# Kernel tuning notes

Measured on AMD Instinct MI355X. Metric: run time of the kernel, lower is better.

Reference implementation:

```python
import math
import jax, jax.numpy as jnp
import numpy as np

EPS = 1e-6
MAX_SCALE_LOG = math.log(100.0)

def rms_norm(x, scale, eps=EPS):
    # x * scale / rms(x), reduction over last dim
    ms = jnp.mean(jnp.square(x), axis=-1, keepdims=True)
    return x * (scale * jax.lax.rsqrt(ms + eps))

def axial_rope_theta(pos, n_heads, d_head, dtype):
    # freqs: linspace in log-space from pi to 10*pi, reshaped to [n_heads, d_head//4]
    f = np.exp(np.linspace(math.log(math.pi), math.log(10.0 * math.pi),
                           n_heads * d_head // 4 + 1)[:-1])
    freqs = jnp.asarray(f.reshape(d_head // 4, n_heads).T, dtype)  # [h, e/4]
    theta_h = pos[:, :, None, 0:1] * freqs  # [n, l, h, e/4]
    theta_w = pos[:, :, None, 1:2] * freqs  # [n, l, h, e/4]
    theta = jnp.concatenate([theta_h, theta_w], axis=-1)  # [n, l, h, e/2]
    return theta.transpose(0, 2, 1, 3)  # [n, h, l, e/2]

def apply_rotary(x, theta):
    d = theta.shape[-1]
    x1, x2, x3 = x[..., :d], x[..., d:2 * d], x[..., 2 * d:]
    cos, sin = jnp.cos(theta), jnp.sin(theta)
    return jnp.concatenate([x1 * cos - x2 * sin, x2 * cos + x1 * sin, x3], axis=-1)

def setup_inputs() -> dict:
    key = jax.random.key(0)
    ks = jax.random.split(key, 8)
    n, l, d_model, d_head = 2, 2048, 1024, 64
    n_heads = d_model // d_head
    x = jax.random.normal(ks[0], (n, l, d_model), jnp.float32)
    pos = jax.random.uniform(ks[1], (n, l, 2), jnp.float32)
    cond = jax.random.normal(ks[2], (n, 1, d_model), jnp.float32)
    # params (torch uses zero-init for w_cond/w_out; small random for a non-degenerate baseline)
    w_cond = jax.random.normal(ks[3], (d_model, d_model), jnp.float32) * 0.02
    w_qkv = jax.random.normal(ks[4], (d_model, 3 * d_model), jnp.float32) * (d_model ** -0.5)
    qk_scale = jnp.full((n_heads,), math.log(10.0), jnp.float32)
    w_out = jax.random.normal(ks[5], (d_model, d_model), jnp.float32) * 0.02
    return {"x": x, "pos": pos, "cond": cond, "w_cond": w_cond,
            "w_qkv": w_qkv, "qk_scale": qk_scale, "w_out": w_out}

def reference(x, pos, cond, w_cond, w_qkv, qk_scale, w_out):
    n, l, d_model = x.shape
    h = qk_scale.shape[0]
    e = d_model // h
    # AdaRMSNorm: scale = linear(cond) + 1
    xn = rms_norm(x, cond @ w_cond + 1.0)
    # QKV projection
    q, k, v = jnp.split(xn @ w_qkv, 3, axis=-1)
    to_heads = lambda t: t.reshape(n, l, h, e).transpose(0, 2, 1, 3)  # [n,h,l,e]
    q, k, v = to_heads(q), to_heads(k), to_heads(v)
    # QKNorm: per-head learned scale, rms over head dim
    s = jnp.exp(0.5 * jnp.minimum(qk_scale, MAX_SCALE_LOG) - 0.25 * math.log(e))
    q = rms_norm(q, s[:, None, None])
    k = rms_norm(k, s[:, None, None])
    # Axial RoPE
    theta = axial_rope_theta(pos, h, e, x.dtype)
    q = apply_rotary(q, theta)
    k = apply_rotary(k, theta)
    # SDPA (no mask)
    attn = jax.nn.softmax(jnp.einsum('nhqe,nhke->nhqk', q, k) / math.sqrt(e), axis=-1)
    o = jnp.einsum('nhqk,nhke->nhqe', attn, v)
    o = o.transpose(0, 2, 1, 3).reshape(n, l, d_model)
    return o @ w_out
```

## Files before the change

### kernel.cpp

```cpp
#include <hip/hip_runtime.h>

typedef unsigned short u16;
typedef unsigned int u32;
typedef short s16x8 __attribute__((ext_vector_type(8)));
typedef short s16x4 __attribute__((ext_vector_type(4)));
typedef float f32x4 __attribute__((ext_vector_type(4)));
typedef float f32x16 __attribute__((ext_vector_type(16)));

#define AS1 __attribute__((address_space(1)))
#define AS3 __attribute__((address_space(3)))

__device__ __forceinline__ float bf2f(u16 u) {
    union { unsigned int i; float f; } x; x.i = ((unsigned int)u) << 16; return x.f;
}
__device__ __forceinline__ u16 f2bf(float f) {
    union { float f; unsigned int i; } x; x.f = f;
    unsigned int r = (x.i + 0x7FFFu + ((x.i >> 16) & 1u)) >> 16;
    return (u16)r;
}
__device__ __forceinline__ void storeOut(u16* p, float v) { *p = f2bf(v); }
__device__ __forceinline__ void storeOut(float* p, float v) { *p = v; }
__device__ __forceinline__ float loadIn(const void* p, size_t i, int isf32) {
    return isf32 ? ((const float*)p)[i] : bf2f(((const u16*)p)[i]);
}
__device__ __forceinline__ float fexp2(float x) {
#if __has_builtin(__builtin_amdgcn_exp2f)
    return __builtin_amdgcn_exp2f(x);
#else
    return exp2f(x);
#endif
}
__device__ __forceinline__ void plswap(u32& a, u32& b) {
#if __has_builtin(__builtin_amdgcn_permlane32_swap)
    const auto r = __builtin_amdgcn_permlane32_swap(a, b, false, false);
    a = (u32)r[0]; b = (u32)r[1];
#else
    asm("v_permlane32_swap_b32 %0, %1" : "+v"(a), "+v"(b));
#endif
}

__global__ __launch_bounds__(256) void detect_dtype(const u16* __restrict__ x,
                                                    int* __restrict__ flag) {
    __shared__ int cnt[4];
    const int tid = threadIdx.x;
    int c = 0;
    #pragma unroll
    for (int i = 0; i < 4; ++i) {
        const u16 u = x[tid * 4 + i];
        const int e = (u >> 7) & 0xFF;
        c += (e >= 101 && e <= 135) ? 1 : 0;
    }
    #pragma unroll
    for (int m = 1; m < 64; m <<= 1) c += __shfl_xor(c, m, 64);
    if ((tid & 63) == 0) cnt[tid >> 6] = c;
    __syncthreads();
    if (tid == 0) {
        const int t = cnt[0] + cnt[1] + cnt[2] + cnt[3];
        *flag = (t < 800) ? 1 : 0;
    }
}

__global__ __launch_bounds__(256) void cond_gemv(const void* __restrict__ cond,
                                                 const void* __restrict__ w,
                                                 float* __restrict__ out,
                                                 const int* __restrict__ flag) {
    const int isf32 = *flag;
    const int d  = blockIdx.x * 256 + threadIdx.x;
    const int n  = blockIdx.y;
    const int k0 = blockIdx.z * 64;
    float acc = 0.f;
    #pragma unroll 8
    for (int k = 0; k < 64; ++k)
        acc += loadIn(cond, n * 1024 + k0 + k, isf32) *
               loadIn(w, (size_t)(k0 + k) * 1024 + d, isf32);
    atomicAdd(out + n * 1024 + d, acc);
}

__global__ __launch_bounds__(256) void rmsnorm_x(const void* __restrict__ x,
                                                 const float* __restrict__ scl,
                                                 u16* __restrict__ xn,
                                                 const int* __restrict__ flag) {
    const int isf32 = *flag;
    const int tok = blockIdx.x;
    const int n = tok >> 11;
    u16* orow = xn + (size_t)tok * 1024;
    const int base = threadIdx.x * 4;
    float f0, f1, f2, f3;
    if (isf32) {
        const float4 v = *(const float4*)((const float*)x + (size_t)tok * 1024 + base);
        f0 = v.x; f1 = v.y; f2 = v.z; f3 = v.w;
    } else {
        s16x4 uv = *(const s16x4*)((const u16*)x + (size_t)tok * 1024 + base);
        f0 = bf2f((u16)uv[0]); f1 = bf2f((u16)uv[1]); f2 = bf2f((u16)uv[2]); f3 = bf2f((u16)uv[3]);
    }
    float ss = f0 * f0 + f1 * f1 + f2 * f2 + f3 * f3;
    #pragma unroll
    for (int m = 1; m < 64; m <<= 1) ss += __shfl_xor(ss, m, 64);
    __shared__ float red[4];
    const int wave = threadIdx.x >> 6, lane = threadIdx.x & 63;
    if (lane == 0) red[wave] = ss;
    __syncthreads();
    float ms = (red[0] + red[1] + red[2] + red[3]) * (1.f / 1024.f);
    float rinv = rsqrtf(ms + 1e-6f);
    orow[base + 0] = f2bf(f0 * (scl[n * 1024 + base + 0] + 1.f) * rinv);
    orow[base + 1] = f2bf(f1 * (scl[n * 1024 + base + 1] + 1.f) * rinv);
    orow[base + 2] = f2bf(f2 * (scl[n * 1024 + base + 2] + 1.f) * rinv);
    orow[base + 3] = f2bf(f3 * (scl[n * 1024 + base + 3] + 1.f) * rinv);
}

__global__ __launch_bounds__(256) void transpose_bf(const void* __restrict__ src,
                                                    u16* __restrict__ dst, int R, int C,
                                                    const int* __restrict__ flag) {
    const int isf32 = *flag;
    __shared__ u16 t[32][33];
    const int c0 = blockIdx.x * 32, r0 = blockIdx.y * 32;
    const int tx = threadIdx.x & 31, ty = threadIdx.x >> 5;
    #pragma unroll
    for (int i = 0; i < 4; ++i)
        t[ty + i * 8][tx] = f2bf(loadIn(src, (size_t)(r0 + ty + i * 8) * C + c0 + tx, isf32));
    __syncthreads();
    #pragma unroll
    for (int i = 0; i < 4; ++i)
        dst[(size_t)(c0 + ty + i * 8) * R + r0 + tx] = t[tx][ty + i * 8];
}

template <typename OutT>
__global__ __launch_bounds__(256) void gemm_bt(const u16* __restrict__ A,
                                               const u16* __restrict__ BT,
                                               OutT* __restrict__ C, int Nn, int K) {
    __shared__ u16 As[128 * 32];
    __shared__ u16 Bs[128 * 32];
    const int tid = threadIdx.x;
    const int wave = tid >> 6, lane = tid & 63;
    const int l15 = lane & 15, quad = lane >> 4;
    const int bm0 = blockIdx.y * 128, bn0 = blockIdx.x * 128;
    const int wr = wave >> 1, wc = wave & 1;
    f32x4 acc[4][4] = {};
    const int srow = lane >> 2;
    const int g = (lane & 3) ^ (srow & 3);
    for (int bk = 0; bk < K; bk += 32) {
        __syncthreads();
        #pragma unroll
        for (int p = 0; p < 2; ++p) {
            const int rowl = p * 64 + wave * 16 + srow;
            const u16* ga = A + (size_t)(bm0 + rowl) * K + bk + g * 8;
            u16* la = As + (p * 64 + wave * 16) * 32;
            __builtin_amdgcn_global_load_lds((const AS1 void*)ga, (AS3 void*)la, 16, 0, 0);
            const u16* gb = BT + (size_t)(bn0 + rowl) * K + bk + g * 8;
            u16* lb = Bs + (p * 64 + wave * 16) * 32;
            __builtin_amdgcn_global_load_lds((const AS1 void*)gb, (AS3 void*)lb, 16, 0, 0);
        }
        __syncthreads();
        s16x8 af[4], bfr[4];
        #pragma unroll
        for (int mt = 0; mt < 4; ++mt) {
            const int r = wr * 64 + mt * 16 + l15;
            af[mt] = *(const s16x8*)(As + r * 32 + ((quad ^ (r & 3)) << 3));
        }
        #pragma unroll
        for (int nt = 0; nt < 4; ++nt) {
            const int r = wc * 64 + nt * 16 + l15;
            bfr[nt] = *(const s16x8*)(Bs + r * 32 + ((quad ^ (r & 3)) << 3));
        }
        #pragma unroll
        for (int mt = 0; mt < 4; ++mt)
            #pragma unroll
            for (int nt = 0; nt < 4; ++nt)
                acc[mt][nt] = __builtin_amdgcn_mfma_f32_16x16x32_bf16(af[mt], bfr[nt], acc[mt][nt], 0, 0, 0);
    }
    #pragma unroll
    for (int mt = 0; mt < 4; ++mt)
        #pragma unroll
        for (int nt = 0; nt < 4; ++nt)
            #pragma unroll
            for (int r = 0; r < 4; ++r) {
                const int row = bm0 + wr * 64 + mt * 16 + quad * 4 + r;
                const int col = bn0 + wc * 64 + nt * 16 + l15;
                storeOut(C + (size_t)row * Nn + col, acc[mt][nt][r]);
            }
}

__global__ __launch_bounds__(256) void qkv_head(const u16* __restrict__ qkv,
                                                const void* __restrict__ pos,
                                                const void* __restrict__ qk_scale,
                                                u16* __restrict__ q_ws,
                                                u16* __restrict__ k_ws,
                                                u16* __restrict__ vtg,
                                                const int* __restrict__ flag) {
    const int isf32 = *flag;
    const int nh = blockIdx.y;
    const int n = nh >> 4, h = nh & 15;
    const int l0 = blockIdx.x * 64;
    const int tid = threadIdx.x;
    const int wave = tid >> 6, lane = tid & 63;

    const float qs = loadIn(qk_scale, h, isf32);
    const float s = __expf(0.5f * fminf(qs, 4.605170186f) - 1.039720771f);
    const float qmul = s * s * 0.125f * 1.44269504089f;
    const int j = lane & 31;
    const float t = (float)((j & 15) * 16 + h);
    const float freq = 3.14159265358979f * __expf(t * (2.302585093f / 256.f));
    const int pj = j >> 4;

    #pragma unroll 2
    for (int it = 0; it < 16; ++it) {
        const int l = l0 + wave * 16 + it;
        const int tok = n * 2048 + l;
        const u16* row = qkv + (size_t)tok * 3072;
        float qv = bf2f(row[h * 64 + lane]);
        float kv = bf2f(row[1024 + h * 64 + lane]);
        float q2 = qv * qv, k2 = kv * kv;
        #pragma unroll
        for (int m = 1; m < 64; m <<= 1) { q2 += __shfl_xor(q2, m, 64); k2 += __shfl_xor(k2, m, 64); }
        float qn = qv * rsqrtf(q2 * (1.f / 64.f) + 1e-6f) * qmul;
        float kn = kv * rsqrtf(k2 * (1.f / 64.f) + 1e-6f);
        const float p = loadIn(pos, tok * 2 + pj, isf32);
        const float th = p * freq;
        const float c = __cosf(th), sn = __sinf(th);
        const float pq = __shfl_xor(qn, 32, 64);
        const float pk = __shfl_xor(kn, 32, 64);
        float qr, kr;
        if (lane < 32) { qr = qn * c - pq * sn; kr = kn * c - pk * sn; }
        else           { qr = qn * c + pq * sn; kr = kn * c + pk * sn; }
        const size_t oidx = ((size_t)nh * 2048 + l) * 64 + lane;
        q_ws[oidx] = f2bf(qr);
        k_ws[oidx] = f2bf(kr);
    }

    __shared__ u16 tbuf[64][65];
    const u16* vsrc = qkv + (size_t)(n * 2048 + l0) * 3072 + 2048 + h * 64;
    #pragma unroll
    for (int it = 0; it < 16; ++it) {
        const int idx = it * 256 + tid;
        const int r = idx >> 6, c = idx & 63;
        tbuf[r][c] = vsrc[(size_t)r * 3072 + c];
    }
    __syncthreads();
    u16* dst = vtg + (size_t)nh * 131072 + l0;
    #pragma unroll
    for (int it = 0; it < 16; ++it) {
        const int idx = it * 256 + tid;
        const int er = idx >> 6, lc = idx & 63;
        dst[(size_t)er * 2048 + lc] = tbuf[lc][er];
    }
}

__global__ __launch_bounds__(256, 2) void attn8(const u16* __restrict__ Q,
                                                const u16* __restrict__ K,
                                                const u16* __restrict__ Vtg,
                                                u16* __restrict__ O) {
    __shared__ u16 Ks[3][64 * 64];
    __shared__ u16 Vt[3][64 * 64];
    const int nh = blockIdx.y;
    const int q0 = blockIdx.x * 128;
    const int tid = threadIdx.x;
    const int wave = tid >> 6, lane = tid & 63;
    const int l31 = lane & 31, h = lane >> 5;
    const size_t hb = (size_t)nh * 2048 * 64;
    const u16* Vbase = Vtg + (size_t)nh * 131072;
    const int drow = lane >> 3;
    const int dch = lane & 7;

    s16x8 qf[4];
    #pragma unroll
    for (int kd = 0; kd < 4; ++kd)
        qf[kd] = *(const s16x8*)(Q + hb + (size_t)(q0 + wave * 32 + l31) * 64 + kd * 16 + h * 8);

    f32x16 Oacc[2] = {};
    float lacc = 0.f;

    auto stage = [&](int tile, int slot) {
        const int kb = tile * 64;
        #pragma unroll
        for (int inst = 0; inst < 2; ++inst) {
            const int row = wave * 16 + inst * 8 + drow;
            const int g = dch ^ (row & 7);
            __builtin_amdgcn_global_load_lds(
                (const AS1 void*)(K + hb + (size_t)(kb + row) * 64 + g * 8),
                (AS3 void*)(Ks[slot] + (wave * 16 + inst * 8) * 64), 16, 0, 0);
            __builtin_amdgcn_global_load_lds(
                (const AS1 void*)(Vbase + (size_t)row * 2048 + kb + g * 8),
                (AS3 void*)(Vt[slot] + (wave * 16 + inst * 8) * 64), 16, 0, 0);
        }
    };

    stage(0, 0);
    stage(1, 1);
    int s0 = 0, s1 = 1, s2 = 2;

    for (int i = 0; i < 32; ++i) {
        asm volatile("s_waitcnt vmcnt(4)" ::: "memory");
        __builtin_amdgcn_sched_barrier(0);
        __builtin_amdgcn_s_barrier();
        stage(i < 30 ? i + 2 : 31, s2);

        const u16* Kt = Ks[s0];
        const u16* Vc = Vt[s0];

        #pragma unroll
        for (int kt = 0; kt < 2; ++kt) {
            f32x16 S;
            #pragma unroll
            for (int jj = 0; jj < 16; ++jj) S[jj] = -15.f;
            const int kr = kt * 32 + l31;
            #pragma unroll
            for (int kd = 0; kd < 4; ++kd) {
                const s16x8 kf = *(const s16x8*)(Kt + kr * 64 + ((((kd << 1) + h) ^ (kr & 7)) << 3));
                S = __builtin_amdgcn_mfma_f32_32x32x16_bf16(kf, qf[kd], S, 0, 0, 0);
            }
            float e[16];
            #pragma unroll
            for (int jj = 0; jj < 16; ++jj) e[jj] = fexp2(S[jj]);
            float rs = 0.f;
            #pragma unroll
            for (int jj = 0; jj < 16; ++jj) rs += e[jj];
            lacc += rs;
            u32 c[8];
            #pragma unroll
            for (int jj = 0; jj < 8; ++jj)
                asm("v_cvt_pk_bf16_f32 %0, %1, %2" : "=v"(c[jj]) : "v"(e[2 * jj]), "v"(e[2 * jj + 1]));
            plswap(c[0], c[2]);
            plswap(c[1], c[3]);
            plswap(c[4], c[6]);
            plswap(c[5], c[7]);
            union { u32 u[4]; s16x8 v; } pfa, pfb;
            pfa.u[0] = c[0]; pfa.u[1] = c[1]; pfa.u[2] = c[2]; pfa.u[3] = c[3];
            pfb.u[0] = c[4]; pfb.u[1] = c[5]; pfb.u[2] = c[6]; pfb.u[3] = c[7];
            #pragma unroll
            for (int et = 0; et < 2; ++et) {
                const int er = et * 32 + l31;
                #pragma unroll
                for (int kdp = 0; kdp < 2; ++kdp) {
                    const int ch = kt * 4 + kdp * 2 + h;
                    const s16x8 vf = *(const s16x8*)(Vc + er * 64 + ((ch ^ (er & 7)) << 3));
                    Oacc[et] = __builtin_amdgcn_mfma_f32_32x32x16_bf16(kdp ? pfb.v : pfa.v, vf, Oacc[et], 0, 0, 0);
                }
            }
        }
        const int t = s0; s0 = s1; s1 = s2; s2 = t;
    }
    asm volatile("s_waitcnt vmcnt(0)" ::: "memory");

    lacc += __shfl_xor(lacc, 32, 64);
    const float linv_l = 1.f / lacc;
    const int n = nh >> 4, hh = nh & 15;
    #pragma unroll
    for (int r = 0; r < 16; ++r) {
        const int ql = (r & 3) + 8 * (r >> 2) + 4 * h;
        const float linv = __shfl(linv_l, ql, 64);
        const int qrow = q0 + wave * 32 + ql;
        #pragma unroll
        for (int et = 0; et < 2; ++et)
            O[((size_t)n * 2048 + qrow) * 1024 + hh * 64 + et * 32 + l31] = f2bf(Oacc[et][r] * linv);
    }
}

extern "C" void kernel_launch(void* const* d_in, const int* in_sizes, int n_in,
                              void* d_out, int out_size, void* d_ws, size_t ws_size,
                              hipStream_t stream) {
    const void* x        = d_in[0];
    const void* pos      = d_in[1];
    const void* cond     = d_in[2];
    const void* w_cond   = d_in[3];
    const void* w_qkv    = d_in[4];
    const void* qk_scale = d_in[5];
    const void* w_out    = d_in[6];

    char* ws = (char*)d_ws;
    constexpr size_t OFS_SCALE = 0;
    constexpr size_t OFS_FLAG  = 8192;
    constexpr size_t OFS_XN    = 16384;
    constexpr size_t OFS_WQKVT = OFS_XN    + 8388608;
    constexpr size_t OFS_WOUTT = OFS_WQKVT + 6291456;
    constexpr size_t OFS_QKV   = OFS_WOUTT + 2097152;
    constexpr size_t OFS_Q     = OFS_QKV   + 25165824;
    constexpr size_t OFS_K     = OFS_Q     + 8388608;
    constexpr size_t OFS_VT    = OFS_K     + 8388608;
    constexpr size_t OFS_O     = OFS_VT    + 8388608;

    float* scale = (float*)(ws + OFS_SCALE);
    int*   flag  = (int*)(ws + OFS_FLAG);
    u16* xn    = (u16*)(ws + OFS_XN);
    u16* wqkvT = (u16*)(ws + OFS_WQKVT);
    u16* woutT = (u16*)(ws + OFS_WOUTT);
    u16* qkv   = (u16*)(ws + OFS_QKV);
    u16* qws   = (u16*)(ws + OFS_Q);
    u16* kws   = (u16*)(ws + OFS_K);
    u16* vtg   = (u16*)(ws + OFS_VT);
    u16* ows   = (u16*)(ws + OFS_O);

    detect_dtype<<<dim3(1), 256, 0, stream>>>((const u16*)x, flag);
    hipMemsetAsync(scale, 0, 2 * 1024 * sizeof(float), stream);
    cond_gemv<<<dim3(4, 2, 16), 256, 0, stream>>>(cond, w_cond, scale, flag);
    rmsnorm_x<<<dim3(4096), 256, 0, stream>>>(x, scale, xn, flag);
    transpose_bf<<<dim3(96, 32), 256, 0, stream>>>(w_qkv, wqkvT, 1024, 3072, flag);
    transpose_bf<<<dim3(32, 32), 256, 0, stream>>>(w_out, woutT, 1024, 1024, flag);
    gemm_bt<u16><<<dim3(24, 32), 256, 0, stream>>>(xn, wqkvT, qkv, 3072, 1024);
    qkv_head<<<dim3(32, 32), 256, 0, stream>>>(qkv, pos, qk_scale, qws, kws, vtg, flag);
    attn8<<<dim3(16, 32), 256, 0, stream>>>(qws, kws, vtg, ows);
    gemm_bt<float><<<dim3(8, 32), 256, 0, stream>>>(ows, woutT, (float*)d_out, 1024, 1024);
}
```

Baseline: 231.6 us.

## Double-buffer 256-key chunks across 8-wave attention blocks with 256 queries

Restructures the attention kernel to run 512 threads per block, each block covering 256 queries, and stages K/V in 256-key chunks with double buffering instead of 64-key tiles with triple buffering. This cuts the number of barrier and wait points per block and shares each K/V load across more query waves. In exchange the block uses much more LDS (about 128 KB), the grid shrinks to 256 blocks, and load latency is less finely overlapped with compute.

Measured after the change: 230.3 us. About the same (-0.6%).

```diff
diff --git a/kernel.cpp b/kernel.cpp
--- a/kernel.cpp
+++ b/kernel.cpp
@@ -245,21 +245,19 @@
     }
 }
 
-__global__ __launch_bounds__(256, 2) void attn8(const u16* __restrict__ Q,
+__global__ __launch_bounds__(512, 2) void attn9(const u16* __restrict__ Q,
                                                 const u16* __restrict__ K,
                                                 const u16* __restrict__ Vtg,
                                                 u16* __restrict__ O) {
-    __shared__ u16 Ks[3][64 * 64];
-    __shared__ u16 Vt[3][64 * 64];
+    __shared__ u16 Ks[2][256 * 64];
+    __shared__ u16 Vt[2][64 * 256];
     const int nh = blockIdx.y;
-    const int q0 = blockIdx.x * 128;
+    const int q0 = blockIdx.x * 256;
     const int tid = threadIdx.x;
     const int wave = tid >> 6, lane = tid & 63;
     const int l31 = lane & 31, h = lane >> 5;
     const size_t hb = (size_t)nh * 2048 * 64;
     const u16* Vbase = Vtg + (size_t)nh * 131072;
-    const int drow = lane >> 3;
-    const int dch = lane & 7;
 
     s16x8 qf[4];
     #pragma unroll
@@ -269,36 +267,44 @@
     f32x16 Oacc[2] = {};
     float lacc = 0.f;
 
-    auto stage = [&](int tile, int slot) {
-        const int kb = tile * 64;
-        #pragma unroll
-        for (int inst = 0; inst < 2; ++inst) {
-            const int row = wave * 16 + inst * 8 + drow;
-            const int g = dch ^ (row & 7);
+    auto stage = [&](int ch, int slot) {
+        const int kb = ch * 256;
+        #pragma unroll
+        for (int r = 0; r < 4; ++r) {
+            const int row = r * 64 + wave * 8 + (lane >> 3);
+            const int g = (lane & 7) ^ (row & 7);
             __builtin_amdgcn_global_load_lds(
                 (const AS1 void*)(K + hb + (size_t)(kb + row) * 64 + g * 8),
-                (AS3 void*)(Ks[slot] + (wave * 16 + inst * 8) * 64), 16, 0, 0);
+                (AS3 void*)(Ks[slot] + (r * 64 + wave * 8) * 64), 16, 0, 0);
+        }
+        #pragma unroll
+        for (int r = 0; r < 4; ++r) {
+            const int er = (r * 8 + wave) * 2 + (lane >> 5);
+            const int g2 = (lane & 31) ^ (er & 7);
             __builtin_amdgcn_global_load_lds(
-                (const AS1 void*)(Vbase + (size_t)row * 2048 + kb + g * 8),
-                (AS3 void*)(Vt[slot] + (wave * 16 + inst * 8) * 64), 16, 0, 0);
+                (const AS1 void*)(Vbase + (size_t)er * 2048 + kb + g2 * 8),
+                (AS3 void*)(Vt[slot] + (r * 8 + wave) * 2 * 256), 16, 0, 0);
         }
     };
 
     stage(0, 0);
-    stage(1, 1);
-    int s0 = 0, s1 = 1, s2 = 2;
-
-    for (int i = 0; i < 32; ++i) {
-        asm volatile("s_waitcnt vmcnt(4)" ::: "memory");
+
+    for (int j = 0; j < 8; ++j) {
+        if (j > 0) __builtin_amdgcn_s_barrier();
+        if (j < 7) {
+            stage(j + 1, (j + 1) & 1);
+            asm volatile("s_waitcnt vmcnt(8)" ::: "memory");
+        } else {
+            asm volatile("s_waitcnt vmcnt(0)" ::: "memory");
+        }
         __builtin_amdgcn_sched_barrier(0);
         __builtin_amdgcn_s_barrier();
-        stage(i < 30 ? i + 2 : 31, s2);
-
-        const u16* Kt = Ks[s0];
-        const u16* Vc = Vt[s0];
-
-        #pragma unroll
-        for (int kt = 0; kt < 2; ++kt) {
+
+        const u16* Kt = Ks[j & 1];
+        const u16* Vc = Vt[j & 1];
+
+        #pragma unroll 2
+        for (int kt = 0; kt < 8; ++kt) {
             f32x16 S;
             #pragma unroll
             for (int jj = 0; jj < 16; ++jj) S[jj] = -15.f;
@@ -332,14 +338,12 @@
                 #pragma unroll
                 for (int kdp = 0; kdp < 2; ++kdp) {
                     const int ch = kt * 4 + kdp * 2 + h;
-                    const s16x8 vf = *(const s16x8*)(Vc + er * 64 + ((ch ^ (er & 7)) << 3));
+                    const s16x8 vf = *(const s16x8*)(Vc + er * 256 + ((ch ^ (er & 7)) << 3));
                     Oacc[et] = __builtin_amdgcn_mfma_f32_32x32x16_bf16(kdp ? pfb.v : pfa.v, vf, Oacc[et], 0, 0, 0);
                 }
             }
         }
-        const int t = s0; s0 = s1; s1 = s2; s2 = t;
-    }
-    asm volatile("s_waitcnt vmcnt(0)" ::: "memory");
+    }
 
     lacc += __shfl_xor(lacc, 32, 64);
     const float linv_l = 1.f / lacc;
@@ -397,6 +401,6 @@
     transpose_bf<<<dim3(32, 32), 256, 0, stream>>>(w_out, woutT, 1024, 1024, flag);
     gemm_bt<u16><<<dim3(24, 32), 256, 0, stream>>>(xn, wqkvT, qkv, 3072, 1024);
     qkv_head<<<dim3(32, 32), 256, 0, stream>>>(qkv, pos, qk_scale, qws, kws, vtg, flag);
-    attn8<<<dim3(16, 32), 256, 0, stream>>>(qws, kws, vtg, ows);
+    attn9<<<dim3(8, 32), 512, 0, stream>>>(qws, kws, vtg, ows);
     gemm_bt<float><<<dim3(8, 32), 256, 0, stream>>>(ows, woutT, (float*)d_out, 1024, 1024);
 }
```
